# Optimization experiments

Hardware: AMD Instinct MI355X
Metric: run time of the kernel (lower is better)

Reference implementation:

```python
import jax, jax.numpy as jnp
import numpy as np

N, DIM, NINC = 2_000_000, 8, 1000


def setup_inputs() -> dict:
    key = jax.random.key(0)
    k_u, k_w = jax.random.split(key)
    u = jax.random.uniform(k_u, (N, DIM), dtype=jnp.float32)
    # Non-uniform but monotone grid per dim over [0, 1]: cumulative of positive random increments.
    w = jax.random.uniform(k_w, (DIM, NINC), dtype=jnp.float32) + 0.5
    cdf = jnp.cumsum(w, axis=1) / jnp.sum(w, axis=1, keepdims=True)  # [dim, ninc], ends at 1
    grid = jnp.concatenate([jnp.zeros((DIM, 1), jnp.float32), cdf], axis=1)  # [dim, ninc+1]
    inc = grid[:, 1:] - grid[:, :-1]  # [dim, ninc]
    return {"u": u, "grid": grid, "inc": inc, "ninc": NINC}


def reference(u, grid, inc, ninc):
    # u: [N, dim]; grid: [dim, ninc+1]; inc: [dim, ninc]
    u_ninc = u * ninc
    iu = jnp.floor(u_ninc).astype(jnp.int32)        # [N, dim] bin index
    du = u_ninc - iu                                 # fractional part within bin
    mask = iu < ninc                                 # points exactly at / beyond upper edge
    iu_c = jnp.clip(iu, 0, ninc - 1)
    # Gather per-dim grid lower edge and increment at each point's bin: [N, dim]
    g = jnp.take_along_axis(grid, iu_c.T, axis=1).T
    h = jnp.take_along_axis(inc, iu_c.T, axis=1).T
    upper = grid[:, ninc][None, :]                   # [1, dim]
    inc_last = inc[:, ninc - 1][None, :]             # [1, dim]
    x = jnp.where(mask, g + h * du, upper)
    fac = jnp.where(mask, h, inc_last) * ninc        # per-dim Jacobian factor
    log_jac = jnp.sum(jnp.log(fac), axis=1)          # [N]
    return x, log_jac
```

## Files before the change

### kernel.cpp

```cpp
#include <hip/hip_runtime.h>
#include <math.h>

#define TPB 1024
#define NDIM 8

typedef float fvec4 __attribute__((ext_vector_type(4)));

__global__ __launch_bounds__(TPB) void vegas_map_kernel(
    const float* __restrict__ u,
    const float* __restrict__ grid,
    float* __restrict__ x_out,
    float* __restrict__ lj_out,
    int n, int gcols, float lj_const)
{
    extern __shared__ float lds_grid[];
    const int ninc = gcols - 1;
    const int gtot4 = (NDIM * gcols) >> 2;

    const fvec4* __restrict__ g4 = (const fvec4*)grid;
    fvec4* lds4 = (fvec4*)lds_grid;
    for (int t = threadIdx.x; t < gtot4; t += TPB)
        lds4[t] = g4[t];
    __syncthreads();

    const float fninc = (float)ninc;
    const fvec4* __restrict__ u4 = (const fvec4*)u;
    fvec4* __restrict__ x4 = (fvec4*)x_out;

    const int stride = gridDim.x * TPB;

    for (int p = blockIdx.x * TPB + threadIdx.x; p < n; p += stride) {
        fvec4 a = u4[2 * p];
        fvec4 b = u4[2 * p + 1];
        float uv[NDIM] = {a.x, a.y, a.z, a.w, b.x, b.y, b.z, b.w};
        float xv[NDIM];
        float prod = 1.0f;

        #pragma unroll
        for (int d = 0; d < NDIM; ++d) {
            float un  = uv[d] * fninc;
            int   iu  = (int)un;
            int   iuc = iu < ninc ? iu : (ninc - 1);
            float du  = un - (float)iuc;
            const float* row = lds_grid + d * gcols;
            float g0 = row[iuc];
            float g1 = row[iuc + 1];
            float h  = g1 - g0;
            xv[d] = g0 + h * du;
            prod *= h;
        }

        fvec4 oa = {xv[0], xv[1], xv[2], xv[3]};
        fvec4 ob = {xv[4], xv[5], xv[6], xv[7]};
        x4[2 * p]     = oa;
        x4[2 * p + 1] = ob;
        lj_out[p] = __logf(prod) + lj_const;
    }
}

extern "C" void kernel_launch(void* const* d_in, const int* in_sizes, int n_in,
                              void* d_out, int out_size, void* d_ws, size_t ws_size,
                              hipStream_t stream) {
    const float* u    = (const float*)d_in[0];
    const float* grid = (const float*)d_in[1];
    const int n     = in_sizes[0] / NDIM;
    const int gcols = in_sizes[1] / NDIM;
    const int ninc  = gcols - 1;

    float* x_out  = (float*)d_out;
    float* lj_out = (float*)d_out + (size_t)n * NDIM;

    const float lj_const = (float)(NDIM * log((double)ninc));

    int blocks = (n + TPB - 1) / TPB;
    if (blocks > 512) blocks = 512;
    size_t lds_bytes = (size_t)NDIM * gcols * sizeof(float);

    vegas_map_kernel<<<blocks, TPB, lds_bytes, stream>>>(u, grid, x_out, lj_out,
                                                         n, gcols, lj_const);
}
```

Baseline: 26.94 us.

## Split each point across two threads, one per half of dimensions

Each thread now handles four dimensions (one float4) instead of all eight, so two adjacent lanes cooperate on one point. The partial Jacobian products are combined with a lane shuffle and only even lanes write the log-Jacobian. This doubles the number of work items and makes global loads and stores fully contiguous float4 per lane, aiming at better coalescing and more memory parallelism. The cost is an extra shuffle, half of the lanes idling during the log and store, and twice the loop iterations per block.

```diff
diff --git a/kernel.cpp b/kernel.cpp
--- a/kernel.cpp
+++ b/kernel.cpp
@@ -11,7 +11,7 @@
     const float* __restrict__ grid,
     float* __restrict__ x_out,
     float* __restrict__ lj_out,
-    int n, int gcols, float lj_const)
+    int nent, int gcols, float lj_const)
 {
     extern __shared__ float lds_grid[];
     const int ninc = gcols - 1;
@@ -27,34 +27,36 @@
     const fvec4* __restrict__ u4 = (const fvec4*)u;
     fvec4* __restrict__ x4 = (fvec4*)x_out;
 
+    const float* rows = lds_grid + (threadIdx.x & 1) * (4 * gcols);
+    const bool is_even = ((threadIdx.x & 1) == 0);
+
     const int stride = gridDim.x * TPB;
-
-    for (int p = blockIdx.x * TPB + threadIdx.x; p < n; p += stride) {
-        fvec4 a = u4[2 * p];
-        fvec4 b = u4[2 * p + 1];
-        float uv[NDIM] = {a.x, a.y, a.z, a.w, b.x, b.y, b.z, b.w};
-        float xv[NDIM];
-        float prod = 1.0f;
+    for (int e = blockIdx.x * TPB + threadIdx.x; e < nent; e += stride) {
+        fvec4 a = u4[e];
+        float uv[4] = {a.x, a.y, a.z, a.w};
+        float xv[4];
+        float pp = 1.0f;
 
         #pragma unroll
-        for (int d = 0; d < NDIM; ++d) {
-            float un  = uv[d] * fninc;
+        for (int k = 0; k < 4; ++k) {
+            float un  = uv[k] * fninc;
             int   iu  = (int)un;
             int   iuc = iu < ninc ? iu : (ninc - 1);
             float du  = un - (float)iuc;
-            const float* row = lds_grid + d * gcols;
+            const float* row = rows + k * gcols;
             float g0 = row[iuc];
             float g1 = row[iuc + 1];
             float h  = g1 - g0;
-            xv[d] = g0 + h * du;
-            prod *= h;
+            xv[k] = g0 + h * du;
+            pp *= h;
         }
 
-        fvec4 oa = {xv[0], xv[1], xv[2], xv[3]};
-        fvec4 ob = {xv[4], xv[5], xv[6], xv[7]};
-        x4[2 * p]     = oa;
-        x4[2 * p + 1] = ob;
-        lj_out[p] = __logf(prod) + lj_const;
+        fvec4 o = {xv[0], xv[1], xv[2], xv[3]};
+        x4[e] = o;
+
+        float po = __shfl_xor(pp, 1);
+        if (is_even)
+            lj_out[e >> 1] = __logf(pp * po) + lj_const;
     }
 }
 
@@ -66,16 +68,17 @@
     const int n     = in_sizes[0] / NDIM;
     const int gcols = in_sizes[1] / NDIM;
     const int ninc  = gcols - 1;
+    const int nent  = 2 * n;
 
     float* x_out  = (float*)d_out;
     float* lj_out = (float*)d_out + (size_t)n * NDIM;
 
     const float lj_const = (float)(NDIM * log((double)ninc));
 
-    int blocks = (n + TPB - 1) / TPB;
+    int blocks = (nent + TPB - 1) / TPB;
     if (blocks > 512) blocks = 512;
     size_t lds_bytes = (size_t)NDIM * gcols * sizeof(float);
 
     vegas_map_kernel<<<blocks, TPB, lds_bytes, stream>>>(u, grid, x_out, lj_out,
-                                                         n, gcols, lj_const);
+                                                         nent, gcols, lj_const);
 }
```

Result: no change. 26.92 us (-0.1%).
